# Optimization experiments

Measured on AMD Instinct MI355X. Metric: run time of the kernel, lower is better.

Reference implementation:

```python
import jax, jax.numpy as jnp
import numpy as np

B, S, D, H, FF = 2, 2048, 512, 8, 2048
DK = D // H
EPS = 1e-5


def layer_norm(x, g, b):
    mu = jnp.mean(x, axis=-1, keepdims=True)
    var = jnp.mean((x - mu) ** 2, axis=-1, keepdims=True)
    return (x - mu) / jnp.sqrt(var + EPS) * g + b


def split_heads(x):  # [B,S,D] -> [B,H,S,DK]
    b, s, _ = x.shape
    return x.reshape(b, s, H, DK).transpose(0, 2, 1, 3)


def merge_heads(x):  # [B,H,S,DK] -> [B,S,D]
    b, h, s, dk = x.shape
    return x.transpose(0, 2, 1, 3).reshape(b, s, h * dk)


def mha(q_in, kv, in_w, in_b, out_w, out_b):
    # torch nn.MultiheadAttention, batch_first, eval mode (no dropout)
    Wq, Wk, Wv = in_w[:D], in_w[D:2 * D], in_w[2 * D:]
    bq, bk, bv = in_b[:D], in_b[D:2 * D], in_b[2 * D:]
    q = split_heads(q_in @ Wq.T + bq)
    k = split_heads(kv @ Wk.T + bk)
    v = split_heads(kv @ Wv.T + bv)
    scores = jnp.einsum('bhqd,bhkd->bhqk', q, k) / jnp.sqrt(jnp.float32(DK))
    attn = jax.nn.softmax(scores, axis=-1)
    out = merge_heads(jnp.einsum('bhqk,bhkd->bhqd', attn, v))
    return out @ out_w.T + out_b


def setup_inputs() -> dict:
    key = jax.random.key(0)
    ks = jax.random.split(key, 32)
    p = lambda k, shape: (jax.random.normal(k, shape, jnp.float32) * 0.02)
    inp = {
        'x_q': jax.random.normal(ks[0], (B, S, D), jnp.float32),
        'x1': jax.random.normal(ks[1], (B, S, D), jnp.float32),
        'x2': jax.random.normal(ks[2], (B, S, D), jnp.float32),
        # causal self-attention projections (no output proj in original)
        'sa_wq': p(ks[3], (D, D)), 'sa_bq': jnp.zeros((D,), jnp.float32),
        'sa_wk': p(ks[4], (D, D)), 'sa_bk': jnp.zeros((D,), jnp.float32),
        'sa_wv': p(ks[5], (D, D)), 'sa_bv': jnp.zeros((D,), jnp.float32),
        'ln1_g': jnp.ones((D,), jnp.float32), 'ln1_b': jnp.zeros((D,), jnp.float32),
        # shared cross-attention (cross_attn used twice in forward)
        'mha_in_w': p(ks[6], (3 * D, D)), 'mha_in_b': jnp.zeros((3 * D,), jnp.float32),
        'mha_out_w': p(ks[7], (D, D)), 'mha_out_b': jnp.zeros((D,), jnp.float32),
        # shared add_norm2 (used twice)
        'ln2_g': jnp.ones((D,), jnp.float32), 'ln2_b': jnp.zeros((D,), jnp.float32),
        # FFN
        'ffn_w1': p(ks[8], (FF, D)), 'ffn_b1': jnp.zeros((FF,), jnp.float32),
        'ffn_w2': p(ks[9], (D, FF)), 'ffn_b2': jnp.zeros((D,), jnp.float32),
        # add_norm3 (final)
        'ln3_g': jnp.ones((D,), jnp.float32), 'ln3_b': jnp.zeros((D,), jnp.float32),
    }
    return inp


def reference(x_q, x1, x2, sa_wq, sa_bq, sa_wk, sa_bk, sa_wv, sa_bv,
              ln1_g, ln1_b, mha_in_w, mha_in_b, mha_out_w, mha_out_b,
              ln2_g, ln2_b, ffn_w1, ffn_b1, ffn_w2, ffn_b2, ln3_g, ln3_b):
    # --- causal self-attention (hand-rolled, masked_fill with -1e9) ---
    q = split_heads(x_q @ sa_wq.T + sa_bq)
    k = split_heads(x_q @ sa_wk.T + sa_bk)
    v = split_heads(x_q @ sa_wv.T + sa_bv)
    scores = jnp.einsum('bhqd,bhkd->bhqk', q, k) / jnp.sqrt(jnp.float32(DK))
    causal = jnp.tril(jnp.ones((S, S), dtype=bool))
    scores = jnp.where(causal[None, None], scores, jnp.float32(-1e9))
    attn = jax.nn.softmax(scores, axis=-1)
    y_sa = merge_heads(jnp.einsum('bhqk,bhkd->bhqd', attn, v))
    y = layer_norm(x_q + y_sa, ln1_g, ln1_b)
    # --- cross-attention 1 (shared weights) + shared add_norm2 ---
    yattn = mha(y, x1, mha_in_w, mha_in_b, mha_out_w, mha_out_b)
    yattn = layer_norm(y + yattn, ln2_g, ln2_b)
    # --- cross-attention 2 (SAME module/weights as cross-attn 1) ---
    yattn2 = mha(yattn, x2, mha_in_w, mha_in_b, mha_out_w, mha_out_b)
    yattn2 = layer_norm(yattn + yattn2, ln2_g, ln2_b)
    # --- FFN + add_norm3 ---
    h = jax.nn.relu(yattn2 @ ffn_w1.T + ffn_b1)
    ff = h @ ffn_w2.T + ffn_b2
    return layer_norm(yattn2 + ff, ln3_g, ln3_b)
```

## Files before the change

### kernel.cpp

```cpp
#include <hip/hip_runtime.h>
#include <hip/hip_bf16.h>

#define S_LEN 2048
#define DMODEL 512
#define NHEAD 8
#define DKH 64
#define FFDIM 2048
#define BATCH 2
#define NROWS (BATCH * S_LEN)

using bf16 = __hip_bfloat16;
typedef __bf16 bf16x8 __attribute__((ext_vector_type(8)));
typedef float floatx4 __attribute__((ext_vector_type(4)));
typedef float floatx16 __attribute__((ext_vector_type(16)));

__device__ inline unsigned short f2bf_bits(float f) {
    union { float f; unsigned u; } c; c.f = f;
    return (unsigned short)((c.u + 0x7FFFu + ((c.u >> 16) & 1u)) >> 16);
}
__device__ inline unsigned pack2bf(float a, float b) {
    return (unsigned)f2bf_bits(a) | ((unsigned)f2bf_bits(b) << 16);
}
__device__ inline unsigned pk2(float a, float b) {
    float2 f; f.x = a; f.y = b;
    __hip_bfloat162 h = __float22bfloat162_rn(f);
    return *(unsigned*)&h;
}

__device__ __forceinline__ void gload_lds16(const bf16* g, bf16* l) {
    __builtin_amdgcn_global_load_lds(
        (const __attribute__((address_space(1))) void*)(const void*)g,
        (__attribute__((address_space(3))) void*)(void*)l, 16, 0, 0);
}

struct CvtSeg { const float* s; bf16* d; int n4; };
struct CvtDesc { CvtSeg seg[12]; };

__launch_bounds__(256)
__global__ void cvt_f32_bf16(CvtDesc desc) {
    const CvtSeg sg = desc.seg[blockIdx.y];
    const int stride = gridDim.x * 256;
    for (int i = blockIdx.x * 256 + threadIdx.x; i < sg.n4; i += stride) {
        const float4 v = ((const float4*)sg.s)[i];
        uint2 o;
        o.x = pack2bf(v.x, v.y);
        o.y = pack2bf(v.z, v.w);
        ((uint2*)sg.d)[i] = o;
    }
}

struct Epi {
    bf16*  outB[3];
    float* outF[3];
    const float* bias[3];
    float scale[3];
    const bf16* A2;
    int a2slab;
    int shift;
    int relu;
};

template <int BM, int BN>
__launch_bounds__(256)
__global__ void gemm2(const bf16* __restrict__ A, const bf16* __restrict__ W,
                      Epi epi, int K)
{
    constexpr int WR = BM / 32;
    constexpr int WC = BN / 32;
    constexpr int SA = BM / 16;
    constexpr int SB = BN / 16;
    constexpr int NG = 2 * (SA + SB);

    __shared__ alignas(16) bf16 As[2][BM][32];
    __shared__ alignas(16) bf16 Bs[2][BN][32];

    const int t = threadIdx.x;
    const int w = t >> 6;
    const int lane = t & 63;
    const int r16 = lane & 15;
    const int quad = lane >> 4;
    const int wm = w >> 1, wn = w & 1;
    const int m0 = blockIdx.x * BM;
    const int n0 = blockIdx.y * BN;

    const bf16* Ause = (epi.A2 && ((n0 >> epi.shift) >= epi.a2slab)) ? epi.A2 : A;

    floatx4 acc[WR][WC];
#pragma unroll
    for (int i = 0; i < WR; i++)
#pragma unroll
        for (int j = 0; j < WC; j++)
#pragma unroll
            for (int e = 0; e < 4; e++) acc[i][j][e] = 0.0f;

    const int grow = lane >> 2;
    const int gcol = (lane & 3) * 8;

    for (int k0 = 0; k0 < K; k0 += 64) {
        __syncthreads();
#pragma unroll
        for (int s = 0; s < NG; s += 4) {
            int sg = s + w;
            int p = 0;
            if (sg >= SA + SB) { p = 1; sg -= SA + SB; }
            const bf16* src;
            bf16* dst;
            if (sg < SA) {
                src = Ause + (size_t)(m0 + sg * 16 + grow) * K + k0 + 32 * p + gcol;
                dst = &As[p][sg * 16][0] + lane * 8;
            } else {
                const int sb = sg - SA;
                src = W + (size_t)(n0 + sb * 16 + grow) * K + k0 + 32 * p + gcol;
                dst = &Bs[p][sb * 16][0] + lane * 8;
            }
            gload_lds16(src, dst);
        }
        __syncthreads();

        bf16x8 af[2][WR], bfr[2][WC];
#pragma unroll
        for (int p = 0; p < 2; p++) {
#pragma unroll
            for (int i = 0; i < WR; i++)
                af[p][i] = *(const bf16x8*)&As[p][wm * (BM / 2) + 16 * i + r16][quad * 8];
#pragma unroll
            for (int j = 0; j < WC; j++)
                bfr[p][j] = *(const bf16x8*)&Bs[p][wn * (BN / 2) + 16 * j + r16][quad * 8];
        }
#pragma unroll
        for (int p = 0; p < 2; p++)
#pragma unroll
            for (int i = 0; i < WR; i++)
#pragma unroll
                for (int j = 0; j < WC; j++)
                    acc[i][j] = __builtin_amdgcn_mfma_f32_16x16x32_bf16(af[p][i], bfr[p][j], acc[i][j], 0, 0, 0);
    }

    const int mask = (1 << epi.shift) - 1;
#pragma unroll
    for (int j = 0; j < WC; j++) {
        const int colb = n0 + wn * (BN / 2) + 16 * j;
        const int sel = __builtin_amdgcn_readfirstlane(colb >> epi.shift);
        const int lcol = (colb & mask) + r16;
        const int ldw = mask + 1;
        const float bv = epi.bias[sel] ? epi.bias[sel][lcol] : 0.0f;
        const float sc = epi.scale[sel];
        bf16* ob = epi.outB[sel];
        float* of = epi.outF[sel];
#pragma unroll
        for (int i = 0; i < WR; i++) {
            const int rowb = m0 + wm * (BM / 2) + 16 * i + 4 * quad;
#pragma unroll
            for (int e = 0; e < 4; e++) {
                float v = (acc[i][j][e] + bv) * sc;
                if (epi.relu) v = fmaxf(v, 0.0f);
                const size_t idx = (size_t)(rowb + e) * ldw + lcol;
                if (of) of[idx] = v;
                if (ob) ob[idx] = __float2bfloat16(v);
            }
        }
    }
}

#define PST 72

__launch_bounds__(512, 2)
__global__ void attn_mfma(const bf16* __restrict__ Qh, const bf16* __restrict__ Kh,
                          const bf16* __restrict__ Vh,
                          float* __restrict__ outF, bf16* __restrict__ outB,
                          int causal)
{
    __shared__ alignas(16) char smem[73728];
    typedef bf16 (*VtT)[64][PST];
    typedef bf16 (*PsT)[32][PST];
    VtT Vt = (VtT)smem;
    PsT Ps = (PsT)(smem + 36864);
    typedef float (*MshT)[2][64][34];
    MshT Msh = (MshT)smem;

    const int t = threadIdx.x;
    const int w = t >> 6;
    const int lane = t & 63;
    const int c32 = lane & 31;
    const int hi = lane >> 5;
    const int pair = t >> 7;
    const int qg = w & 1;
    const int pl = t & 127;
    const int bh = blockIdx.y;
    const int b = bh >> 3, h = bh & 7;
    const int q0 = blockIdx.x * 64;
    const size_t rowbase = (size_t)b * S_LEN;
    const int hoff = h * DKH;

    bf16x8 qf[4];
    {
        const bf16* qp = Qh + (rowbase + q0 + 32 * qg + c32) * DMODEL + hoff + 8 * hi;
#pragma unroll
        for (int tt = 0; tt < 4; tt++) qf[tt] = *(const bf16x8*)(qp + 16 * tt);
    }

    floatx16 o0, o1;
#pragma unroll
    for (int e = 0; e < 16; e++) { o0[e] = 0.0f; o1[e] = 0.0f; }
    float m = -3e38f, l = 0.0f;

    const int rq = pl & 15;
    const int c8 = ((pl >> 4) & 7) * 8;

    const int nchunk = causal ? (q0 / 64 + 1) : (S_LEN / 64);
    const int nIter = (nchunk + 3) >> 2;

    bf16x8 kf0[4], kf1[4];
    if (pair < nchunk) {
        const bf16* kp = Kh + (rowbase + pair * 64 + c32) * DMODEL + hoff + 8 * hi;
#pragma unroll
        for (int tt = 0; tt < 4; tt++) {
            kf0[tt] = *(const bf16x8*)(kp + 16 * tt);
            kf1[tt] = *(const bf16x8*)(kp + (size_t)32 * DMODEL + 16 * tt);
        }
    }

    for (int it = 0; it < nIter; it++) {
        const int ch = 4 * it + pair;
        const bool active = ch < nchunk;
        const int kb = ch * 64;
        __syncthreads();
        if (active) {
            union { uint4 u; unsigned short s[8]; } r0, r1, r2, r3;
            const bf16* vb = Vh + (rowbase + kb + 4 * rq) * DMODEL + hoff + c8;
            r0.u = *(const uint4*)(vb);
            r1.u = *(const uint4*)(vb + DMODEL);
            r2.u = *(const uint4*)(vb + 2 * DMODEL);
            r3.u = *(const uint4*)(vb + 3 * DMODEL);
#pragma unroll
            for (int j = 0; j < 8; j++) {
                ushort4 pk = { r0.s[j], r1.s[j], r2.s[j], r3.s[j] };
                *(ushort4*)&Vt[pair][c8 + j][4 * rq] = pk;
            }
        }

        if (active) {
            floatx16 s0, s1;
#pragma unroll
            for (int e = 0; e < 16; e++) { s0[e] = 0.0f; s1[e] = 0.0f; }
            __builtin_amdgcn_s_setprio(1);
#pragma unroll
            for (int tt = 0; tt < 4; tt++) {
                s0 = __builtin_amdgcn_mfma_f32_32x32x16_bf16(kf0[tt], qf[tt], s0, 0, 0, 0);
                s1 = __builtin_amdgcn_mfma_f32_32x32x16_bf16(kf1[tt], qf[tt], s1, 0, 0, 0);
            }
            __builtin_amdgcn_s_setprio(0);

            const int chn = ch + 4;
            if (chn < nchunk) {
                const bf16* kp = Kh + (rowbase + chn * 64 + c32) * DMODEL + hoff + 8 * hi;
#pragma unroll
                for (int tt = 0; tt < 4; tt++) {
                    kf0[tt] = *(const bf16x8*)(kp + 16 * tt);
                    kf1[tt] = *(const bf16x8*)(kp + (size_t)32 * DMODEL + 16 * tt);
                }
            }

            if (causal && kb == q0) {
                const int qq = 32 * qg + c32;
#pragma unroll
                for (int r = 0; r < 16; r++) {
                    const int kl = (r & 3) + 8 * (r >> 2) + 4 * hi;
                    if (kl > qq) s0[r] = -3e38f;
                    if (kl + 32 > qq) s1[r] = -3e38f;
                }
            }

            float mc = -3e38f;
#pragma unroll
            for (int r = 0; r < 16; r++) mc = fmaxf(mc, fmaxf(s0[r], s1[r]));
            mc = fmaxf(mc, __shfl_xor(mc, 32, 64));

            float alpha = 1.0f;
            if (!__all(mc <= m + 8.0f)) {
                const float mold = m;
                m = fmaxf(m, mc);
                alpha = __builtin_amdgcn_exp2f(mold - m);
#pragma unroll
                for (int r = 0; r < 16; r++) {
                    const float a = __shfl(alpha, (r & 3) + 8 * (r >> 2) + 4 * hi, 64);
                    o0[r] *= a; o1[r] *= a;
                }
            }

            float lc = 0.0f;
#pragma unroll
            for (int g = 0; g < 4; g++) {
                float p0 = __builtin_amdgcn_exp2f(s0[4 * g + 0] - m);
                float p1 = __builtin_amdgcn_exp2f(s0[4 * g + 1] - m);
                float p2 = __builtin_amdgcn_exp2f(s0[4 * g + 2] - m);
                float p3 = __builtin_amdgcn_exp2f(s0[4 * g + 3] - m);
                lc += (p0 + p1) + (p2 + p3);
                uint2 pw; pw.x = pk2(p0, p1); pw.y = pk2(p2, p3);
                *(uint2*)&Ps[w][c32][8 * g + 4 * hi] = pw;
                p0 = __builtin_amdgcn_exp2f(s1[4 * g + 0] - m);
                p1 = __builtin_amdgcn_exp2f(s1[4 * g + 1] - m);
                p2 = __builtin_amdgcn_exp2f(s1[4 * g + 2] - m);
                p3 = __builtin_amdgcn_exp2f(s1[4 * g + 3] - m);
                lc += (p0 + p1) + (p2 + p3);
                uint2 pw1; pw1.x = pk2(p0, p1); pw1.y = pk2(p2, p3);
                *(uint2*)&Ps[w][c32][32 + 8 * g + 4 * hi] = pw1;
            }
            lc += __shfl_xor(lc, 32, 64);
            l = l * alpha + lc;
        }

        __syncthreads();

        if (active) {
            __builtin_amdgcn_s_setprio(1);
#pragma unroll
            for (int tt = 0; tt < 4; tt++) {
                const bf16x8 pf = *(const bf16x8*)&Ps[w][c32][16 * tt + 8 * hi];
                const bf16x8 v0 = *(const bf16x8*)&Vt[pair][c32][16 * tt + 8 * hi];
                const bf16x8 v1 = *(const bf16x8*)&Vt[pair][32 + c32][16 * tt + 8 * hi];
                o0 = __builtin_amdgcn_mfma_f32_32x32x16_bf16(pf, v0, o0, 0, 0, 0);
                o1 = __builtin_amdgcn_mfma_f32_32x32x16_bf16(pf, v1, o1, 0, 0, 0);
            }
            __builtin_amdgcn_s_setprio(0);
        }
    }

    __syncthreads();
    if (pair & 1) {
        float* dst = &Msh[pair >> 1][qg][lane][0];
        dst[0] = m; dst[1] = l;
#pragma unroll
        for (int r = 0; r < 16; r++) { dst[2 + r] = o0[r]; dst[18 + r] = o1[r]; }
    }
    __syncthreads();
    if ((pair & 1) == 0) {
        const float* src = &Msh[pair >> 1][qg][lane][0];
        const float m_b = src[0], l_b = src[1];
        const float mt = fmaxf(m, m_b);
        const float sA = __builtin_amdgcn_exp2f(m - mt);
        const float sB = __builtin_amdgcn_exp2f(m_b - mt);
        l = l * sA + l_b * sB;
        m = mt;
#pragma unroll
        for (int r = 0; r < 16; r++) {
            const int ql = (r & 3) + 8 * (r >> 2) + 4 * hi;
            const float sAr = __shfl(sA, ql, 64);
            const float sBr = __shfl(sB, ql, 64);
            o0[r] = o0[r] * sAr + src[2 + r] * sBr;
            o1[r] = o1[r] * sAr + src[18 + r] * sBr;
        }
        if (pair == 2) {
            float* dst = &Msh[1][qg][lane][0];
            dst[0] = m; dst[1] = l;
#pragma unroll
            for (int r = 0; r < 16; r++) { dst[2 + r] = o0[r]; dst[18 + r] = o1[r]; }
        }
    }
    __syncthreads();
    if (pair == 0) {
        const float* src = &Msh[1][qg][lane][0];
        const float m_b = src[0], l_b = src[1];
        const float mt = fmaxf(m, m_b);
        const float sA = __builtin_amdgcn_exp2f(m - mt);
        const float sB = __builtin_amdgcn_exp2f(m_b - mt);
        const float lt = l * sA + l_b * sB;
#pragma unroll
        for (int r = 0; r < 16; r++) {
            const int ql = (r & 3) + 8 * (r >> 2) + 4 * hi;
            const float sAr = __shfl(sA, ql, 64);
            const float sBr = __shfl(sB, ql, 64);
            const float li = 1.0f / __shfl(lt, ql, 64);
            const float v0 = (o0[r] * sAr + src[2 + r] * sBr) * li;
            const float v1 = (o1[r] * sAr + src[18 + r] * sBr) * li;
            const size_t idx = (rowbase + q0 + 32 * qg + ql) * DMODEL + hoff + c32;
            if (outF) { outF[idx] = v0; outF[idx + 32] = v1; }
            if (outB) { outB[idx] = __float2bfloat16(v0); outB[idx + 32] = __float2bfloat16(v1); }
        }
    }
}

__launch_bounds__(256)
__global__ void ln_kernel(const float* __restrict__ xmain,
                          const float* __restrict__ resF, const bf16* __restrict__ resB,
                          const float* __restrict__ g, const float* __restrict__ bb,
                          float* __restrict__ outF, bf16* __restrict__ outB)
{
    const int row = blockIdx.x;
    const int t = threadIdx.x;
    const size_t base = (size_t)row * DMODEL;

    float x0 = xmain[base + t];
    float x1 = xmain[base + t + 256];
    if (resF) { x0 += resF[base + t]; x1 += resF[base + t + 256]; }
    if (resB) { x0 += __bfloat162float(resB[base + t]); x1 += __bfloat162float(resB[base + t + 256]); }

    __shared__ float sred[4];
    float s = x0 + x1;
#pragma unroll
    for (int off = 32; off > 0; off >>= 1) s += __shfl_down(s, off);
    if ((t & 63) == 0) sred[t >> 6] = s;
    __syncthreads();
    const float mu = (sred[0] + sred[1] + sred[2] + sred[3]) * (1.0f / DMODEL);

    const float d0 = x0 - mu, d1 = x1 - mu;
    float sv = d0 * d0 + d1 * d1;
#pragma unroll
    for (int off = 32; off > 0; off >>= 1) sv += __shfl_down(sv, off);
    __syncthreads();
    if ((t & 63) == 0) sred[t >> 6] = sv;
    __syncthreads();
    const float var = (sred[0] + sred[1] + sred[2] + sred[3]) * (1.0f / DMODEL);
    const float rstd = rsqrtf(var + 1e-5f);

    const float y0 = d0 * rstd * g[t] + bb[t];
    const float y1 = d1 * rstd * g[t + 256] + bb[t + 256];
    if (outF) { outF[base + t] = y0; outF[base + t + 256] = y1; }
    if (outB) { outB[base + t] = __float2bfloat16(y0); outB[base + t + 256] = __float2bfloat16(y1); }
}

extern "C" void kernel_launch(void* const* d_in, const int* in_sizes, int n_in,
                              void* d_out, int out_size, void* d_ws, size_t ws_size,
                              hipStream_t stream)
{
    const float* x_q       = (const float*)d_in[0];
    const float* x1        = (const float*)d_in[1];
    const float* x2        = (const float*)d_in[2];
    const float* sa_wq     = (const float*)d_in[3];
    const float* sa_bq     = (const float*)d_in[4];
    const float* sa_wk     = (const float*)d_in[5];
    const float* sa_bk     = (const float*)d_in[6];
    const float* sa_wv     = (const float*)d_in[7];
    const float* sa_bv     = (const float*)d_in[8];
    const float* ln1_g     = (const float*)d_in[9];
    const float* ln1_b     = (const float*)d_in[10];
    const float* mha_in_w  = (const float*)d_in[11];
    const float* mha_in_b  = (const float*)d_in[12];
    const float* mha_out_w = (const float*)d_in[13];
    const float* mha_out_b = (const float*)d_in[14];
    const float* ln2_g     = (const float*)d_in[15];
    const float* ln2_b     = (const float*)d_in[16];
    const float* ffn_w1    = (const float*)d_in[17];
    const float* ffn_b1    = (const float*)d_in[18];
    const float* ffn_w2    = (const float*)d_in[19];
    const float* ffn_b2    = (const float*)d_in[20];
    const float* ln3_g     = (const float*)d_in[21];
    const float* ln3_b     = (const float*)d_in[22];

    char* ws = (char*)d_ws;
    const size_t MB = 1024 * 1024;
    const size_t KB = 1024;
    bf16*  q16  = (bf16*)(ws + 0 * MB);
    bf16*  k16  = (bf16*)(ws + 4 * MB);
    bf16*  v16  = (bf16*)(ws + 8 * MB);
    bf16*  a16  = (bf16*)(ws + 12 * MB);
    float* tmp  = (float*)(ws + 16 * MB);
    bf16*  y16  = (bf16*)(ws + 24 * MB);
    bf16*  ya16 = (bf16*)(ws + 28 * MB);
    bf16*  ya2  = (bf16*)(ws + 32 * MB);
    bf16*  xq16 = (bf16*)(ws + 36 * MB);
    bf16*  x116 = (bf16*)(ws + 40 * MB);
    bf16*  x216 = (bf16*)(ws + 44 * MB);
    bf16*  w_sa_qkv = (bf16*)(ws + 48 * MB);
    bf16*  w_in   = (bf16*)(ws + 49 * MB + 512 * KB);
    bf16*  w_out  = (bf16*)(ws + 51 * MB);
    bf16*  w_f1   = (bf16*)(ws + 51 * MB + 512 * KB);
    bf16*  w_f2   = (bf16*)(ws + 53 * MB + 512 * KB);
    bf16*  h16    = (bf16*)(ws + 0 * MB);

    const int DD = DMODEL * DMODEL;
    CvtDesc cd;
    cd.seg[0]  = { x_q,       xq16,        (NROWS * DMODEL) / 4 };
    cd.seg[1]  = { x1,        x116,        (NROWS * DMODEL) / 4 };
    cd.seg[2]  = { x2,        x216,        (NROWS * DMODEL) / 4 };
    cd.seg[3]  = { sa_wq,     w_sa_qkv,           DD / 4 };
    cd.seg[4]  = { sa_wk,     w_sa_qkv + DD,      DD / 4 };
    cd.seg[5]  = { sa_wv,     w_sa_qkv + 2 * DD,  DD / 4 };
    cd.seg[6]  = { mha_in_w,  w_in,   3 * DD / 4 };
    cd.seg[7]  = { mha_out_w, w_out,  DD / 4 };
    cd.seg[8]  = { ffn_w1,    w_f1,   (FFDIM * DMODEL) / 4 };
    cd.seg[9]  = { ffn_w2,    w_f2,   (FFDIM * DMODEL) / 4 };
    cd.seg[10] = { x_q,       xq16,   0 };
    cd.seg[11] = { x_q,       xq16,   0 };
    cvt_f32_bf16<<<dim3(64, 10), 256, 0, stream>>>(cd);

    const dim3 blk(256);
    const dim3 ablk(512);
    const dim3 agrid(S_LEN / 64, BATCH * NHEAD);

    const float QSC = 0.125f * 1.44269504088896f;

    Epi eQKV = {};
    eQKV.outB[0] = q16; eQKV.outB[1] = k16; eQKV.outB[2] = v16;
    eQKV.bias[0] = sa_bq; eQKV.bias[1] = sa_bk; eQKV.bias[2] = sa_bv;
    eQKV.scale[0] = QSC; eQKV.scale[1] = 1.0f; eQKV.scale[2] = 1.0f;
    eQKV.shift = 9;

    Epi eX1 = {};
    eX1.outB[0] = q16; eX1.outB[1] = k16; eX1.outB[2] = v16;
    eX1.bias[0] = mha_in_b; eX1.bias[1] = mha_in_b + DMODEL; eX1.bias[2] = mha_in_b + 2 * DMODEL;
    eX1.scale[0] = QSC; eX1.scale[1] = 1.0f; eX1.scale[2] = 1.0f;
    eX1.A2 = x116; eX1.a2slab = 1; eX1.shift = 9;

    Epi eX2 = eX1;
    eX2.A2 = x216;

    Epi eOut = {};
    eOut.outF[0] = tmp; eOut.bias[0] = mha_out_b; eOut.scale[0] = 1.0f; eOut.shift = 9;

    Epi eF1 = {};
    eF1.outB[0] = h16; eF1.bias[0] = ffn_b1; eF1.scale[0] = 1.0f;
    eF1.shift = 11; eF1.relu = 1;

    Epi eF2 = {};
    eF2.outF[0] = tmp; eF2.bias[0] = ffn_b2; eF2.scale[0] = 1.0f; eF2.shift = 9;

    gemm2<64, 64><<<dim3(64, 24), blk, 0, stream>>>(xq16, w_sa_qkv, eQKV, DMODEL);
    attn_mfma<<<agrid, ablk, 0, stream>>>(q16, k16, v16, tmp, nullptr, 1);
    ln_kernel<<<NROWS, blk, 0, stream>>>(tmp, x_q, nullptr, ln1_g, ln1_b, nullptr, y16);

    gemm2<64, 64><<<dim3(64, 24), blk, 0, stream>>>(y16, w_in, eX1, DMODEL);
    attn_mfma<<<agrid, ablk, 0, stream>>>(q16, k16, v16, nullptr, a16, 0);
    gemm2<64, 64><<<dim3(64, 8), blk, 0, stream>>>(a16, w_out, eOut, DMODEL);
    ln_kernel<<<NROWS, blk, 0, stream>>>(tmp, nullptr, y16, ln2_g, ln2_b, nullptr, ya16);

    gemm2<64, 64><<<dim3(64, 24), blk, 0, stream>>>(ya16, w_in, eX2, DMODEL);
    attn_mfma<<<agrid, ablk, 0, stream>>>(q16, k16, v16, nullptr, a16, 0);
    gemm2<64, 64><<<dim3(64, 8), blk, 0, stream>>>(a16, w_out, eOut, DMODEL);
    ln_kernel<<<NROWS, blk, 0, stream>>>(tmp, nullptr, ya16, ln2_g, ln2_b, nullptr, ya2);

    gemm2<128, 128><<<dim3(32, 16), blk, 0, stream>>>(ya2, w_f1, eF1, DMODEL);
    gemm2<64, 64><<<dim3(64, 8), blk, 0, stream>>>(h16, w_f2, eF2, FFDIM);
    ln_kernel<<<NROWS, blk, 0, stream>>>(tmp, nullptr, ya2, ln3_g, ln3_b, (float*)d_out, nullptr);
}
```

Before: 440.6 us.

## Write V transposed from QKV GEMM epilogue and read it directly in attention

The QKV projection epilogue now stores V in a per-batch transposed [D, S] layout, so the attention kernel can load V fragments straight from global memory into registers. This removes the per-chunk LDS transpose of V, the V shared-memory buffer, and both block-wide barriers in the attention loop, letting each wave pair proceed independently. The cost is strided, uncoalesced 2-byte scattered stores in the GEMM epilogue and V fragment loads from global/L2 issued inside the loop, which are not prefetched ahead like K.

```diff
diff --git a/kernel.cpp b/kernel.cpp
--- a/kernel.cpp
+++ b/kernel.cpp
@@ -58,6 +58,7 @@
     int a2slab;
     int shift;
     int relu;
+    int vtransSel;
 };
 
 template <int BM, int BN>
@@ -150,13 +151,24 @@
 #pragma unroll
         for (int i = 0; i < WR; i++) {
             const int rowb = m0 + wm * (BM / 2) + 16 * i + 4 * quad;
-#pragma unroll
-            for (int e = 0; e < 4; e++) {
-                float v = (acc[i][j][e] + bv) * sc;
-                if (epi.relu) v = fmaxf(v, 0.0f);
-                const size_t idx = (size_t)(rowb + e) * ldw + lcol;
-                if (of) of[idx] = v;
-                if (ob) ob[idx] = __float2bfloat16(v);
+            if (sel == epi.vtransSel) {
+#pragma unroll
+                for (int e = 0; e < 4; e++) {
+                    const int row = rowb + e;
+                    const float v = (acc[i][j][e] + bv) * sc;
+                    const size_t tidx = ((size_t)(row >> 11) * DMODEL + lcol) * (size_t)S_LEN
+                                      + (row & (S_LEN - 1));
+                    ob[tidx] = __float2bfloat16(v);
+                }
+            } else {
+#pragma unroll
+                for (int e = 0; e < 4; e++) {
+                    float v = (acc[i][j][e] + bv) * sc;
+                    if (epi.relu) v = fmaxf(v, 0.0f);
+                    const size_t idx = (size_t)(rowb + e) * ldw + lcol;
+                    if (of) of[idx] = v;
+                    if (ob) ob[idx] = __float2bfloat16(v);
+                }
             }
         }
     }
@@ -166,15 +178,13 @@
 
 __launch_bounds__(512, 2)
 __global__ void attn_mfma(const bf16* __restrict__ Qh, const bf16* __restrict__ Kh,
-                          const bf16* __restrict__ Vh,
+                          const bf16* __restrict__ VTh,
                           float* __restrict__ outF, bf16* __restrict__ outB,
                           int causal)
 {
-    __shared__ alignas(16) char smem[73728];
-    typedef bf16 (*VtT)[64][PST];
+    __shared__ alignas(16) char smem[36864];
     typedef bf16 (*PsT)[32][PST];
-    VtT Vt = (VtT)smem;
-    PsT Ps = (PsT)(smem + 36864);
+    PsT Ps = (PsT)smem;
     typedef float (*MshT)[2][64][34];
     MshT Msh = (MshT)smem;
 
@@ -183,9 +193,8 @@
     const int lane = t & 63;
     const int c32 = lane & 31;
     const int hi = lane >> 5;
-    const int pair = t >> 7;
+    const int pair = w >> 1;
     const int qg = w & 1;
-    const int pl = t & 127;
     const int bh = blockIdx.y;
     const int b = bh >> 3, h = bh & 7;
     const int q0 = blockIdx.x * 64;
@@ -204,11 +213,10 @@
     for (int e = 0; e < 16; e++) { o0[e] = 0.0f; o1[e] = 0.0f; }
     float m = -3e38f, l = 0.0f;
 
-    const int rq = pl & 15;
-    const int c8 = ((pl >> 4) & 7) * 8;
-
     const int nchunk = causal ? (q0 / 64 + 1) : (S_LEN / 64);
-    const int nIter = (nchunk + 3) >> 2;
+
+    const bf16* vb0 = VTh + ((size_t)b * DMODEL + hoff + c32) * S_LEN;
+    const bf16* vb1 = VTh + ((size_t)b * DMODEL + hoff + 32 + c32) * S_LEN;
 
     bf16x8 kf0[4], kf1[4];
     if (pair < nchunk) {
@@ -220,110 +228,92 @@
         }
     }
 
-    for (int it = 0; it < nIter; it++) {
-        const int ch = 4 * it + pair;
-        const bool active = ch < nchunk;
+    for (int ch = pair; ch < nchunk; ch += 4) {
         const int kb = ch * 64;
-        __syncthreads();
-        if (active) {
-            union { uint4 u; unsigned short s[8]; } r0, r1, r2, r3;
-            const bf16* vb = Vh + (rowbase + kb + 4 * rq) * DMODEL + hoff + c8;
-            r0.u = *(const uint4*)(vb);
-            r1.u = *(const uint4*)(vb + DMODEL);
-            r2.u = *(const uint4*)(vb + 2 * DMODEL);
-            r3.u = *(const uint4*)(vb + 3 * DMODEL);
-#pragma unroll
-            for (int j = 0; j < 8; j++) {
-                ushort4 pk = { r0.s[j], r1.s[j], r2.s[j], r3.s[j] };
-                *(ushort4*)&Vt[pair][c8 + j][4 * rq] = pk;
+
+        floatx16 s0, s1;
+#pragma unroll
+        for (int e = 0; e < 16; e++) { s0[e] = 0.0f; s1[e] = 0.0f; }
+        __builtin_amdgcn_s_setprio(1);
+#pragma unroll
+        for (int tt = 0; tt < 4; tt++) {
+            s0 = __builtin_amdgcn_mfma_f32_32x32x16_bf16(kf0[tt], qf[tt], s0, 0, 0, 0);
+            s1 = __builtin_amdgcn_mfma_f32_32x32x16_bf16(kf1[tt], qf[tt], s1, 0, 0, 0);
+        }
+        __builtin_amdgcn_s_setprio(0);
+
+        if (ch + 4 < nchunk) {
+            const bf16* kp = Kh + (rowbase + (ch + 4) * 64 + c32) * DMODEL + hoff + 8 * hi;
+#pragma unroll
+            for (int tt = 0; tt < 4; tt++) {
+                kf0[tt] = *(const bf16x8*)(kp + 16 * tt);
+                kf1[tt] = *(const bf16x8*)(kp + (size_t)32 * DMODEL + 16 * tt);
             }
         }
 
-        if (active) {
-            floatx16 s0, s1;
-#pragma unroll
-            for (int e = 0; e < 16; e++) { s0[e] = 0.0f; s1[e] = 0.0f; }
-            __builtin_amdgcn_s_setprio(1);
-#pragma unroll
-            for (int tt = 0; tt < 4; tt++) {
-                s0 = __builtin_amdgcn_mfma_f32_32x32x16_bf16(kf0[tt], qf[tt], s0, 0, 0, 0);
-                s1 = __builtin_amdgcn_mfma_f32_32x32x16_bf16(kf1[tt], qf[tt], s1, 0, 0, 0);
+        if (causal && kb == q0) {
+            const int qq = 32 * qg + c32;
+#pragma unroll
+            for (int r = 0; r < 16; r++) {
+                const int kl = (r & 3) + 8 * (r >> 2) + 4 * hi;
+                if (kl > qq) s0[r] = -3e38f;
+                if (kl + 32 > qq) s1[r] = -3e38f;
             }
-            __builtin_amdgcn_s_setprio(0);
-
-            const int chn = ch + 4;
-            if (chn < nchunk) {
-                const bf16* kp = Kh + (rowbase + chn * 64 + c32) * DMODEL + hoff + 8 * hi;
-#pragma unroll
-                for (int tt = 0; tt < 4; tt++) {
-                    kf0[tt] = *(const bf16x8*)(kp + 16 * tt);
-                    kf1[tt] = *(const bf16x8*)(kp + (size_t)32 * DMODEL + 16 * tt);
-                }
+        }
+
+        float mc = -3e38f;
+#pragma unroll
+        for (int r = 0; r < 16; r++) mc = fmaxf(mc, fmaxf(s0[r], s1[r]));
+        mc = fmaxf(mc, __shfl_xor(mc, 32, 64));
+
+        float alpha = 1.0f;
+        if (!__all(mc <= m + 8.0f)) {
+            const float mold = m;
+            m = fmaxf(m, mc);
+            alpha = __builtin_amdgcn_exp2f(mold - m);
+#pragma unroll
+            for (int r = 0; r < 16; r++) {
+                const float a = __shfl(alpha, (r & 3) + 8 * (r >> 2) + 4 * hi, 64);
+                o0[r] *= a; o1[r] *= a;
             }
-
-            if (causal && kb == q0) {
-                const int qq = 32 * qg + c32;
-#pragma unroll
-                for (int r = 0; r < 16; r++) {
-                    const int kl = (r & 3) + 8 * (r >> 2) + 4 * hi;
-                    if (kl > qq) s0[r] = -3e38f;
-                    if (kl + 32 > qq) s1[r] = -3e38f;
-                }
-            }
-
-            float mc = -3e38f;
-#pragma unroll
-            for (int r = 0; r < 16; r++) mc = fmaxf(mc, fmaxf(s0[r], s1[r]));
-            mc = fmaxf(mc, __shfl_xor(mc, 32, 64));
-
-            float alpha = 1.0f;
-            if (!__all(mc <= m + 8.0f)) {
-                const float mold = m;
-                m = fmaxf(m, mc);
-                alpha = __builtin_amdgcn_exp2f(mold - m);
-#pragma unroll
-                for (int r = 0; r < 16; r++) {
-                    const float a = __shfl(alpha, (r & 3) + 8 * (r >> 2) + 4 * hi, 64);
-                    o0[r] *= a; o1[r] *= a;
-                }
-            }
-
-            float lc = 0.0f;
-#pragma unroll
-            for (int g = 0; g < 4; g++) {
-                float p0 = __builtin_amdgcn_exp2f(s0[4 * g + 0] - m);
-                float p1 = __builtin_amdgcn_exp2f(s0[4 * g + 1] - m);
-                float p2 = __builtin_amdgcn_exp2f(s0[4 * g + 2] - m);
-                float p3 = __builtin_amdgcn_exp2f(s0[4 * g + 3] - m);
-                lc += (p0 + p1) + (p2 + p3);
-                uint2 pw; pw.x = pk2(p0, p1); pw.y = pk2(p2, p3);
-                *(uint2*)&Ps[w][c32][8 * g + 4 * hi] = pw;
-                p0 = __builtin_amdgcn_exp2f(s1[4 * g + 0] - m);
-                p1 = __builtin_amdgcn_exp2f(s1[4 * g + 1] - m);
-                p2 = __builtin_amdgcn_exp2f(s1[4 * g + 2] - m);
-                p3 = __builtin_amdgcn_exp2f(s1[4 * g + 3] - m);
-                lc += (p0 + p1) + (p2 + p3);
-                uint2 pw1; pw1.x = pk2(p0, p1); pw1.y = pk2(p2, p3);
-                *(uint2*)&Ps[w][c32][32 + 8 * g + 4 * hi] = pw1;
-            }
-            lc += __shfl_xor(lc, 32, 64);
-            l = l * alpha + lc;
-        }
-
-        __syncthreads();
-
-        if (active) {
-            __builtin_amdgcn_s_setprio(1);
-#pragma unroll
-            for (int tt = 0; tt < 4; tt++) {
-                const bf16x8 pf = *(const bf16x8*)&Ps[w][c32][16 * tt + 8 * hi];
-                const bf16x8 v0 = *(const bf16x8*)&Vt[pair][c32][16 * tt + 8 * hi];
-                const bf16x8 v1 = *(const bf16x8*)&Vt[pair][32 + c32][16 * tt + 8 * hi];
-                o0 = __builtin_amdgcn_mfma_f32_32x32x16_bf16(pf, v0, o0, 0, 0, 0);
-                o1 = __builtin_amdgcn_mfma_f32_32x32x16_bf16(pf, v1, o1, 0, 0, 0);
-            }
-            __builtin_amdgcn_s_setprio(0);
-        }
+        }
+
+        float lc = 0.0f;
+#pragma unroll
+        for (int g = 0; g < 4; g++) {
+            float p0 = __builtin_amdgcn_exp2f(s0[4 * g + 0] - m);
+            float p1 = __builtin_amdgcn_exp2f(s0[4 * g + 1] - m);
+            float p2 = __builtin_amdgcn_exp2f(s0[4 * g + 2] - m);
+            float p3 = __builtin_amdgcn_exp2f(s0[4 * g + 3] - m);
+            lc += (p0 + p1) + (p2 + p3);
+            uint2 pw; pw.x = pk2(p0, p1); pw.y = pk2(p2, p3);
+            *(uint2*)&Ps[w][c32][8 * g + 4 * hi] = pw;
+            p0 = __builtin_amdgcn_exp2f(s1[4 * g + 0] - m);
+            p1 = __builtin_amdgcn_exp2f(s1[4 * g + 1] - m);
+            p2 = __builtin_amdgcn_exp2f(s1[4 * g + 2] - m);
+            p3 = __builtin_amdgcn_exp2f(s1[4 * g + 3] - m);
+            lc += (p0 + p1) + (p2 + p3);
+            uint2 pw1; pw1.x = pk2(p0, p1); pw1.y = pk2(p2, p3);
+            *(uint2*)&Ps[w][c32][32 + 8 * g + 4 * hi] = pw1;
+        }
+        lc += __shfl_xor(lc, 32, 64);
+        l = l * alpha + lc;
+
+        bf16x8 vf0[4], vf1[4];
+#pragma unroll
+        for (int tt = 0; tt < 4; tt++) {
+            vf0[tt] = *(const bf16x8*)(vb0 + kb + 16 * tt + 8 * hi);
+            vf1[tt] = *(const bf16x8*)(vb1 + kb + 16 * tt + 8 * hi);
+        }
+
+        __builtin_amdgcn_s_setprio(1);
+#pragma unroll
+        for (int tt = 0; tt < 4; tt++) {
+            const bf16x8 pf = *(const bf16x8*)&Ps[w][c32][16 * tt + 8 * hi];
+            o0 = __builtin_amdgcn_mfma_f32_32x32x16_bf16(pf, vf0[tt], o0, 0, 0, 0);
+            o1 = __builtin_amdgcn_mfma_f32_32x32x16_bf16(pf, vf1[tt], o1, 0, 0, 0);
+        }
+        __builtin_amdgcn_s_setprio(0);
     }
 
     __syncthreads();
@@ -452,7 +442,7 @@
     const size_t KB = 1024;
     bf16*  q16  = (bf16*)(ws + 0 * MB);
     bf16*  k16  = (bf16*)(ws + 4 * MB);
-    bf16*  v16  = (bf16*)(ws + 8 * MB);
+    bf16*  vT16 = (bf16*)(ws + 8 * MB);
     bf16*  a16  = (bf16*)(ws + 12 * MB);
     float* tmp  = (float*)(ws + 16 * MB);
     bf16*  y16  = (bf16*)(ws + 24 * MB);
@@ -491,41 +481,43 @@
     const float QSC = 0.125f * 1.44269504088896f;
 
     Epi eQKV = {};
-    eQKV.outB[0] = q16; eQKV.outB[1] = k16; eQKV.outB[2] = v16;
+    eQKV.outB[0] = q16; eQKV.outB[1] = k16; eQKV.outB[2] = vT16;
     eQKV.bias[0] = sa_bq; eQKV.bias[1] = sa_bk; eQKV.bias[2] = sa_bv;
     eQKV.scale[0] = QSC; eQKV.scale[1] = 1.0f; eQKV.scale[2] = 1.0f;
-    eQKV.shift = 9;
+    eQKV.shift = 9; eQKV.vtransSel = 2;
 
     Epi eX1 = {};
-    eX1.outB[0] = q16; eX1.outB[1] = k16; eX1.outB[2] = v16;
+    eX1.outB[0] = q16; eX1.outB[1] = k16; eX1.outB[2] = vT16;
     eX1.bias[0] = mha_in_b; eX1.bias[1] = mha_in_b + DMODEL; eX1.bias[2] = mha_in_b + 2 * DMODEL;
     eX1.scale[0] = QSC; eX1.scale[1] = 1.0f; eX1.scale[2] = 1.0f;
-    eX1.A2 = x116; eX1.a2slab = 1; eX1.shift = 9;
+    eX1.A2 = x116; eX1.a2slab = 1; eX1.shift = 9; eX1.vtransSel = 2;
 
     Epi eX2 = eX1;
     eX2.A2 = x216;
 
     Epi eOut = {};
     eOut.outF[0] = tmp; eOut.bias[0] = mha_out_b; eOut.scale[0] = 1.0f; eOut.shift = 9;
+    eOut.vtransSel = -1;
 
     Epi eF1 = {};
     eF1.outB[0] = h16; eF1.bias[0] = ffn_b1; eF1.scale[0] = 1.0f;
-    eF1.shift = 11; eF1.relu = 1;
+    eF1.shift = 11; eF1.relu = 1; eF1.vtransSel = -1;
 
     Epi eF2 = {};
     eF2.outF[0] = tmp; eF2.bias[0] = ffn_b2; eF2.scale[0] = 1.0f; eF2.shift = 9;
+    eF2.vtransSel = -1;
 
     gemm2<64, 64><<<dim3(64, 24), blk, 0, stream>>>(xq16, w_sa_qkv, eQKV, DMODEL);
-    attn_mfma<<<agrid, ablk, 0, stream>>>(q16, k16, v16, tmp, nullptr, 1);
+    attn_mfma<<<agrid, ablk, 0, stream>>>(q16, k16, vT16, tmp, nullptr, 1);
     ln_kernel<<<NROWS, blk, 0, stream>>>(tmp, x_q, nullptr, ln1_g, ln1_b, nullptr, y16);
 
     gemm2<64, 64><<<dim3(64, 24), blk, 0, stream>>>(y16, w_in, eX1, DMODEL);
-    attn_mfma<<<agrid, ablk, 0, stream>>>(q16, k16, v16, nullptr, a16, 0);
+    attn_mfma<<<agrid, ablk, 0, stream>>>(q16, k16, vT16, nullptr, a16, 0);
     gemm2<64, 64><<<dim3(64, 8), blk, 0, stream>>>(a16, w_out, eOut, DMODEL);
     ln_kernel<<<NROWS, blk, 0, stream>>>(tmp, nullptr, y16, ln2_g, ln2_b, nullptr, ya16);
 
     gemm2<64, 64><<<dim3(64, 24), blk, 0, stream>>>(ya16, w_in, eX2, DMODEL);
-    attn_mfma<<<agrid, ablk, 0, stream>>>(q16, k16, v16, nullptr, a16, 0);
+    attn_mfma<<<agrid, ablk, 0, stream>>>(q16, k16, vT16, nullptr, a16, 0);
     gemm2<64, 64><<<dim3(64, 8), blk, 0, stream>>>(a16, w_out, eOut, DMODEL);
     ln_kernel<<<NROWS, blk, 0, stream>>>(tmp, nullptr, ya16, ln2_g, ln2_b, nullptr, ya2);
 
```

Measured after the change: 477.6 us. 1.08x slower.

## Stage K tiles through LDS with coalesced loads instead of register prefetch

Applied to the files above, without the earlier changes.

The attention kernel now loads each 64-row K chunk with coalesced 16-byte global loads into a shared-memory tile, then reads the MFMA fragments back from LDS. The tile shares space with the P buffer, and V moves to the second half of shared memory. This targets the strided per-lane global K fragment loads. In exchange it drops the register prefetch of the next K chunk that overlapped with the softmax work, and adds barriers to each iteration while removing the one before the PV MFMA.

```diff
diff --git a/kernel.cpp b/kernel.cpp
--- a/kernel.cpp
+++ b/kernel.cpp
@@ -171,10 +171,12 @@
                           int causal)
 {
     __shared__ alignas(16) char smem[73728];
+    typedef bf16 (*KsT)[64][PST];
+    typedef bf16 (*PsT)[32][PST];
     typedef bf16 (*VtT)[64][PST];
-    typedef bf16 (*PsT)[32][PST];
-    VtT Vt = (VtT)smem;
-    PsT Ps = (PsT)(smem + 36864);
+    KsT Ks = (KsT)smem;
+    PsT Ps = (PsT)smem;
+    VtT Vt = (VtT)(smem + 36864);
     typedef float (*MshT)[2][64][34];
     MshT Msh = (MshT)smem;
 
@@ -206,26 +208,29 @@
 
     const int rq = pl & 15;
     const int c8 = ((pl >> 4) & 7) * 8;
+    const int ku = pl & 7;
+    const int kr0 = pl >> 3;
 
     const int nchunk = causal ? (q0 / 64 + 1) : (S_LEN / 64);
     const int nIter = (nchunk + 3) >> 2;
-
-    bf16x8 kf0[4], kf1[4];
-    if (pair < nchunk) {
-        const bf16* kp = Kh + (rowbase + pair * 64 + c32) * DMODEL + hoff + 8 * hi;
-#pragma unroll
-        for (int tt = 0; tt < 4; tt++) {
-            kf0[tt] = *(const bf16x8*)(kp + 16 * tt);
-            kf1[tt] = *(const bf16x8*)(kp + (size_t)32 * DMODEL + 16 * tt);
-        }
-    }
 
     for (int it = 0; it < nIter; it++) {
         const int ch = 4 * it + pair;
         const bool active = ch < nchunk;
         const int kb = ch * 64;
         __syncthreads();
+
         if (active) {
+            const bf16* kpg = Kh + (rowbase + kb + kr0) * DMODEL + hoff + ku * 8;
+            uint4 ka = *(const uint4*)(kpg);
+            uint4 kbv = *(const uint4*)(kpg + (size_t)16 * DMODEL);
+            uint4 kc = *(const uint4*)(kpg + (size_t)32 * DMODEL);
+            uint4 kd = *(const uint4*)(kpg + (size_t)48 * DMODEL);
+            *(uint4*)&Ks[pair][kr0     ][ku * 8] = ka;
+            *(uint4*)&Ks[pair][kr0 + 16][ku * 8] = kbv;
+            *(uint4*)&Ks[pair][kr0 + 32][ku * 8] = kc;
+            *(uint4*)&Ks[pair][kr0 + 48][ku * 8] = kd;
+
             union { uint4 u; unsigned short s[8]; } r0, r1, r2, r3;
             const bf16* vb = Vh + (rowbase + kb + 4 * rq) * DMODEL + hoff + c8;
             r0.u = *(const uint4*)(vb);
@@ -239,6 +244,19 @@
             }
         }
 
+        __syncthreads();
+
+        bf16x8 kf0[4], kf1[4];
+        if (active) {
+#pragma unroll
+            for (int tt = 0; tt < 4; tt++) {
+                kf0[tt] = *(const bf16x8*)&Ks[pair][c32][16 * tt + 8 * hi];
+                kf1[tt] = *(const bf16x8*)&Ks[pair][32 + c32][16 * tt + 8 * hi];
+            }
+        }
+
+        __syncthreads();
+
         if (active) {
             floatx16 s0, s1;
 #pragma unroll
@@ -250,16 +268,6 @@
                 s1 = __builtin_amdgcn_mfma_f32_32x32x16_bf16(kf1[tt], qf[tt], s1, 0, 0, 0);
             }
             __builtin_amdgcn_s_setprio(0);
-
-            const int chn = ch + 4;
-            if (chn < nchunk) {
-                const bf16* kp = Kh + (rowbase + chn * 64 + c32) * DMODEL + hoff + 8 * hi;
-#pragma unroll
-                for (int tt = 0; tt < 4; tt++) {
-                    kf0[tt] = *(const bf16x8*)(kp + 16 * tt);
-                    kf1[tt] = *(const bf16x8*)(kp + (size_t)32 * DMODEL + 16 * tt);
-                }
-            }
 
             if (causal && kb == q0) {
                 const int qq = 32 * qg + c32;
@@ -308,11 +316,7 @@
             }
             lc += __shfl_xor(lc, 32, 64);
             l = l * alpha + lc;
-        }
-
-        __syncthreads();
-
-        if (active) {
+
             __builtin_amdgcn_s_setprio(1);
 #pragma unroll
             for (int tt = 0; tt < 4; tt++) {
```

Measured after the change: 434.6 us. No clear change (-1.4%).

## Shrink attention blocks to 32 queries and make per-wave KV loop barrier-free

Applied to the files above, without the earlier changes.

The attention kernel now uses 256-thread blocks covering 32 query rows instead of 512 threads covering 64. Each wave owns its own key chunks and a private transposed-V buffer, so the per-iteration block-wide __syncthreads calls go away. V is staged in two 32-row halves, interleaved with the PV MFMAs, and the causal mask is applied only on each query tile's last chunk. The grid doubles and LDS use halves, which should raise occupancy and tighten causal load balance, at the cost of K/V being reloaded for twice as many query tiles.

```diff
diff --git a/kernel.cpp b/kernel.cpp
--- a/kernel.cpp
+++ b/kernel.cpp
@@ -163,19 +163,20 @@
 }
 
 #define PST 72
-
-__launch_bounds__(512, 2)
+#define PSTH 36
+
+__launch_bounds__(256, 4)
 __global__ void attn_mfma(const bf16* __restrict__ Qh, const bf16* __restrict__ Kh,
                           const bf16* __restrict__ Vh,
                           float* __restrict__ outF, bf16* __restrict__ outB,
                           int causal)
 {
-    __shared__ alignas(16) char smem[73728];
-    typedef bf16 (*VtT)[64][PST];
+    __shared__ alignas(16) char smem[36864];
+    typedef bf16 (*VtT)[64][PSTH];
     typedef bf16 (*PsT)[32][PST];
     VtT Vt = (VtT)smem;
-    PsT Ps = (PsT)(smem + 36864);
-    typedef float (*MshT)[2][64][34];
+    PsT Ps = (PsT)(smem + 18432);
+    typedef float (*MshT)[64][34];
     MshT Msh = (MshT)smem;
 
     const int t = threadIdx.x;
@@ -183,18 +184,15 @@
     const int lane = t & 63;
     const int c32 = lane & 31;
     const int hi = lane >> 5;
-    const int pair = t >> 7;
-    const int qg = w & 1;
-    const int pl = t & 127;
     const int bh = blockIdx.y;
     const int b = bh >> 3, h = bh & 7;
-    const int q0 = blockIdx.x * 64;
+    const int q0 = blockIdx.x * 32;
     const size_t rowbase = (size_t)b * S_LEN;
     const int hoff = h * DKH;
 
     bf16x8 qf[4];
     {
-        const bf16* qp = Qh + (rowbase + q0 + 32 * qg + c32) * DMODEL + hoff + 8 * hi;
+        const bf16* qp = Qh + (rowbase + q0 + c32) * DMODEL + hoff + 8 * hi;
 #pragma unroll
         for (int tt = 0; tt < 4; tt++) qf[tt] = *(const bf16x8*)(qp + 16 * tt);
     }
@@ -204,15 +202,14 @@
     for (int e = 0; e < 16; e++) { o0[e] = 0.0f; o1[e] = 0.0f; }
     float m = -3e38f, l = 0.0f;
 
-    const int rq = pl & 15;
-    const int c8 = ((pl >> 4) & 7) * 8;
+    const int vq = lane & 7;
+    const int vd = (lane >> 3) * 8;
 
     const int nchunk = causal ? (q0 / 64 + 1) : (S_LEN / 64);
-    const int nIter = (nchunk + 3) >> 2;
 
     bf16x8 kf0[4], kf1[4];
-    if (pair < nchunk) {
-        const bf16* kp = Kh + (rowbase + pair * 64 + c32) * DMODEL + hoff + 8 * hi;
+    if (w < nchunk) {
+        const bf16* kp = Kh + (rowbase + w * 64 + c32) * DMODEL + hoff + 8 * hi;
 #pragma unroll
         for (int tt = 0; tt < 4; tt++) {
             kf0[tt] = *(const bf16x8*)(kp + 16 * tt);
@@ -220,122 +217,142 @@
         }
     }
 
-    for (int it = 0; it < nIter; it++) {
-        const int ch = 4 * it + pair;
-        const bool active = ch < nchunk;
+    for (int ch = w; ch < nchunk; ch += 4) {
         const int kb = ch * 64;
-        __syncthreads();
-        if (active) {
+
+        floatx16 s0, s1;
+#pragma unroll
+        for (int e = 0; e < 16; e++) { s0[e] = 0.0f; s1[e] = 0.0f; }
+        __builtin_amdgcn_s_setprio(1);
+#pragma unroll
+        for (int tt = 0; tt < 4; tt++) {
+            s0 = __builtin_amdgcn_mfma_f32_32x32x16_bf16(kf0[tt], qf[tt], s0, 0, 0, 0);
+            s1 = __builtin_amdgcn_mfma_f32_32x32x16_bf16(kf1[tt], qf[tt], s1, 0, 0, 0);
+        }
+        __builtin_amdgcn_s_setprio(0);
+
+        const bf16* vb0 = Vh + (rowbase + kb + 4 * vq) * DMODEL + hoff + vd;
+        uint4 va0 = *(const uint4*)(vb0);
+        uint4 va1 = *(const uint4*)(vb0 + DMODEL);
+        uint4 va2 = *(const uint4*)(vb0 + 2 * DMODEL);
+        uint4 va3 = *(const uint4*)(vb0 + 3 * DMODEL);
+
+        if (causal && ch == nchunk - 1) {
+            const int qq = q0 + c32;
+#pragma unroll
+            for (int r = 0; r < 16; r++) {
+                const int kl = kb + (r & 3) + 8 * (r >> 2) + 4 * hi;
+                if (kl > qq) s0[r] = -3e38f;
+                if (kl + 32 > qq) s1[r] = -3e38f;
+            }
+        }
+
+        float mc = -3e38f;
+#pragma unroll
+        for (int r = 0; r < 16; r++) mc = fmaxf(mc, fmaxf(s0[r], s1[r]));
+        mc = fmaxf(mc, __shfl_xor(mc, 32, 64));
+
+        float alpha = 1.0f;
+        if (!__all(mc <= m + 8.0f)) {
+            const float mold = m;
+            m = fmaxf(m, mc);
+            alpha = __builtin_amdgcn_exp2f(mold - m);
+#pragma unroll
+            for (int r = 0; r < 16; r++) {
+                const float a = __shfl(alpha, (r & 3) + 8 * (r >> 2) + 4 * hi, 64);
+                o0[r] *= a; o1[r] *= a;
+            }
+        }
+
+        float lc = 0.0f;
+#pragma unroll
+        for (int g = 0; g < 4; g++) {
+            float p0 = __builtin_amdgcn_exp2f(s0[4 * g + 0] - m);
+            float p1 = __builtin_amdgcn_exp2f(s0[4 * g + 1] - m);
+            float p2 = __builtin_amdgcn_exp2f(s0[4 * g + 2] - m);
+            float p3 = __builtin_amdgcn_exp2f(s0[4 * g + 3] - m);
+            lc += (p0 + p1) + (p2 + p3);
+            uint2 pw; pw.x = pk2(p0, p1); pw.y = pk2(p2, p3);
+            *(uint2*)&Ps[w][c32][8 * g + 4 * hi] = pw;
+            p0 = __builtin_amdgcn_exp2f(s1[4 * g + 0] - m);
+            p1 = __builtin_amdgcn_exp2f(s1[4 * g + 1] - m);
+            p2 = __builtin_amdgcn_exp2f(s1[4 * g + 2] - m);
+            p3 = __builtin_amdgcn_exp2f(s1[4 * g + 3] - m);
+            lc += (p0 + p1) + (p2 + p3);
+            uint2 pw1; pw1.x = pk2(p0, p1); pw1.y = pk2(p2, p3);
+            *(uint2*)&Ps[w][c32][32 + 8 * g + 4 * hi] = pw1;
+        }
+        lc += __shfl_xor(lc, 32, 64);
+        l = l * alpha + lc;
+
+        if (ch + 4 < nchunk) {
+            const bf16* kp = Kh + (rowbase + (ch + 4) * 64 + c32) * DMODEL + hoff + 8 * hi;
+#pragma unroll
+            for (int tt = 0; tt < 4; tt++) {
+                kf0[tt] = *(const bf16x8*)(kp + 16 * tt);
+                kf1[tt] = *(const bf16x8*)(kp + (size_t)32 * DMODEL + 16 * tt);
+            }
+        }
+
+        {
             union { uint4 u; unsigned short s[8]; } r0, r1, r2, r3;
-            const bf16* vb = Vh + (rowbase + kb + 4 * rq) * DMODEL + hoff + c8;
-            r0.u = *(const uint4*)(vb);
-            r1.u = *(const uint4*)(vb + DMODEL);
-            r2.u = *(const uint4*)(vb + 2 * DMODEL);
-            r3.u = *(const uint4*)(vb + 3 * DMODEL);
+            r0.u = va0; r1.u = va1; r2.u = va2; r3.u = va3;
 #pragma unroll
             for (int j = 0; j < 8; j++) {
                 ushort4 pk = { r0.s[j], r1.s[j], r2.s[j], r3.s[j] };
-                *(ushort4*)&Vt[pair][c8 + j][4 * rq] = pk;
-            }
-        }
-
-        if (active) {
-            floatx16 s0, s1;
-#pragma unroll
-            for (int e = 0; e < 16; e++) { s0[e] = 0.0f; s1[e] = 0.0f; }
-            __builtin_amdgcn_s_setprio(1);
-#pragma unroll
-            for (int tt = 0; tt < 4; tt++) {
-                s0 = __builtin_amdgcn_mfma_f32_32x32x16_bf16(kf0[tt], qf[tt], s0, 0, 0, 0);
-                s1 = __builtin_amdgcn_mfma_f32_32x32x16_bf16(kf1[tt], qf[tt], s1, 0, 0, 0);
-            }
-            __builtin_amdgcn_s_setprio(0);
-
-            const int chn = ch + 4;
-            if (chn < nchunk) {
-                const bf16* kp = Kh + (rowbase + chn * 64 + c32) * DMODEL + hoff + 8 * hi;
-#pragma unroll
-                for (int tt = 0; tt < 4; tt++) {
-                    kf0[tt] = *(const bf16x8*)(kp + 16 * tt);
-                    kf1[tt] = *(const bf16x8*)(kp + (size_t)32 * DMODEL + 16 * tt);
-                }
-            }
-
-            if (causal && kb == q0) {
-                const int qq = 32 * qg + c32;
-#pragma unroll
-                for (int r = 0; r < 16; r++) {
-                    const int kl = (r & 3) + 8 * (r >> 2) + 4 * hi;
-                    if (kl > qq) s0[r] = -3e38f;
-                    if (kl + 32 > qq) s1[r] = -3e38f;
-                }
-            }
-
-            float mc = -3e38f;
-#pragma unroll
-            for (int r = 0; r < 16; r++) mc = fmaxf(mc, fmaxf(s0[r], s1[r]));
-            mc = fmaxf(mc, __shfl_xor(mc, 32, 64));
-
-            float alpha = 1.0f;
-            if (!__all(mc <= m + 8.0f)) {
-                const float mold = m;
-                m = fmaxf(m, mc);
-                alpha = __builtin_amdgcn_exp2f(mold - m);
-#pragma unroll
-                for (int r = 0; r < 16; r++) {
-                    const float a = __shfl(alpha, (r & 3) + 8 * (r >> 2) + 4 * hi, 64);
-                    o0[r] *= a; o1[r] *= a;
-                }
-            }
-
-            float lc = 0.0f;
-#pragma unroll
-            for (int g = 0; g < 4; g++) {
-                float p0 = __builtin_amdgcn_exp2f(s0[4 * g + 0] - m);
-                float p1 = __builtin_amdgcn_exp2f(s0[4 * g + 1] - m);
-                float p2 = __builtin_amdgcn_exp2f(s0[4 * g + 2] - m);
-                float p3 = __builtin_amdgcn_exp2f(s0[4 * g + 3] - m);
-                lc += (p0 + p1) + (p2 + p3);
-                uint2 pw; pw.x = pk2(p0, p1); pw.y = pk2(p2, p3);
-                *(uint2*)&Ps[w][c32][8 * g + 4 * hi] = pw;
-                p0 = __builtin_amdgcn_exp2f(s1[4 * g + 0] - m);
-                p1 = __builtin_amdgcn_exp2f(s1[4 * g + 1] - m);
-                p2 = __builtin_amdgcn_exp2f(s1[4 * g + 2] - m);
-                p3 = __builtin_amdgcn_exp2f(s1[4 * g + 3] - m);
-                lc += (p0 + p1) + (p2 + p3);
-                uint2 pw1; pw1.x = pk2(p0, p1); pw1.y = pk2(p2, p3);
-                *(uint2*)&Ps[w][c32][32 + 8 * g + 4 * hi] = pw1;
-            }
-            lc += __shfl_xor(lc, 32, 64);
-            l = l * alpha + lc;
-        }
-
-        __syncthreads();
-
-        if (active) {
-            __builtin_amdgcn_s_setprio(1);
-#pragma unroll
-            for (int tt = 0; tt < 4; tt++) {
-                const bf16x8 pf = *(const bf16x8*)&Ps[w][c32][16 * tt + 8 * hi];
-                const bf16x8 v0 = *(const bf16x8*)&Vt[pair][c32][16 * tt + 8 * hi];
-                const bf16x8 v1 = *(const bf16x8*)&Vt[pair][32 + c32][16 * tt + 8 * hi];
-                o0 = __builtin_amdgcn_mfma_f32_32x32x16_bf16(pf, v0, o0, 0, 0, 0);
-                o1 = __builtin_amdgcn_mfma_f32_32x32x16_bf16(pf, v1, o1, 0, 0, 0);
-            }
-            __builtin_amdgcn_s_setprio(0);
-        }
+                *(ushort4*)&Vt[w][vd + j][4 * vq] = pk;
+            }
+        }
+
+        const bf16* vb1 = Vh + (rowbase + kb + 32 + 4 * vq) * DMODEL + hoff + vd;
+        uint4 vc0 = *(const uint4*)(vb1);
+        uint4 vc1 = *(const uint4*)(vb1 + DMODEL);
+        uint4 vc2 = *(const uint4*)(vb1 + 2 * DMODEL);
+        uint4 vc3 = *(const uint4*)(vb1 + 3 * DMODEL);
+
+        __builtin_amdgcn_s_setprio(1);
+#pragma unroll
+        for (int tt = 0; tt < 2; tt++) {
+            const bf16x8 pf = *(const bf16x8*)&Ps[w][c32][16 * tt + 8 * hi];
+            const bf16x8 v0 = *(const bf16x8*)&Vt[w][c32][16 * tt + 8 * hi];
+            const bf16x8 v1 = *(const bf16x8*)&Vt[w][32 + c32][16 * tt + 8 * hi];
+            o0 = __builtin_amdgcn_mfma_f32_32x32x16_bf16(pf, v0, o0, 0, 0, 0);
+            o1 = __builtin_amdgcn_mfma_f32_32x32x16_bf16(pf, v1, o1, 0, 0, 0);
+        }
+        __builtin_amdgcn_s_setprio(0);
+
+        {
+            union { uint4 u; unsigned short s[8]; } r0, r1, r2, r3;
+            r0.u = vc0; r1.u = vc1; r2.u = vc2; r3.u = vc3;
+#pragma unroll
+            for (int j = 0; j < 8; j++) {
+                ushort4 pk = { r0.s[j], r1.s[j], r2.s[j], r3.s[j] };
+                *(ushort4*)&Vt[w][vd + j][4 * vq] = pk;
+            }
+        }
+
+        __builtin_amdgcn_s_setprio(1);
+#pragma unroll
+        for (int tt = 2; tt < 4; tt++) {
+            const bf16x8 pf = *(const bf16x8*)&Ps[w][c32][16 * tt + 8 * hi];
+            const bf16x8 v0 = *(const bf16x8*)&Vt[w][c32][16 * (tt - 2) + 8 * hi];
+            const bf16x8 v1 = *(const bf16x8*)&Vt[w][32 + c32][16 * (tt - 2) + 8 * hi];
+            o0 = __builtin_amdgcn_mfma_f32_32x32x16_bf16(pf, v0, o0, 0, 0, 0);
+            o1 = __builtin_amdgcn_mfma_f32_32x32x16_bf16(pf, v1, o1, 0, 0, 0);
+        }
+        __builtin_amdgcn_s_setprio(0);
     }
 
     __syncthreads();
-    if (pair & 1) {
-        float* dst = &Msh[pair >> 1][qg][lane][0];
+    if (w & 1) {
+        float* dst = &Msh[w >> 1][lane][0];
         dst[0] = m; dst[1] = l;
 #pragma unroll
         for (int r = 0; r < 16; r++) { dst[2 + r] = o0[r]; dst[18 + r] = o1[r]; }
     }
     __syncthreads();
-    if ((pair & 1) == 0) {
-        const float* src = &Msh[pair >> 1][qg][lane][0];
+    if ((w & 1) == 0) {
+        const float* src = &Msh[w >> 1][lane][0];
         const float m_b = src[0], l_b = src[1];
         const float mt = fmaxf(m, m_b);
         const float sA = __builtin_amdgcn_exp2f(m - mt);
@@ -350,16 +367,16 @@
             o0[r] = o0[r] * sAr + src[2 + r] * sBr;
             o1[r] = o1[r] * sAr + src[18 + r] * sBr;
         }
-        if (pair == 2) {
-            float* dst = &Msh[1][qg][lane][0];
+        if (w == 2) {
+            float* dst = &Msh[1][lane][0];
             dst[0] = m; dst[1] = l;
 #pragma unroll
             for (int r = 0; r < 16; r++) { dst[2 + r] = o0[r]; dst[18 + r] = o1[r]; }
         }
     }
     __syncthreads();
-    if (pair == 0) {
-        const float* src = &Msh[1][qg][lane][0];
+    if (w == 0) {
+        const float* src = &Msh[1][lane][0];
         const float m_b = src[0], l_b = src[1];
         const float mt = fmaxf(m, m_b);
         const float sA = __builtin_amdgcn_exp2f(m - mt);
@@ -373,7 +390,7 @@
             const float li = 1.0f / __shfl(lt, ql, 64);
             const float v0 = (o0[r] * sAr + src[2 + r] * sBr) * li;
             const float v1 = (o1[r] * sAr + src[18 + r] * sBr) * li;
-            const size_t idx = (rowbase + q0 + 32 * qg + ql) * DMODEL + hoff + c32;
+            const size_t idx = (rowbase + q0 + ql) * DMODEL + hoff + c32;
             if (outF) { outF[idx] = v0; outF[idx + 32] = v1; }
             if (outB) { outB[idx] = __float2bfloat16(v0); outB[idx + 32] = __float2bfloat16(v1); }
         }
@@ -485,8 +502,8 @@
     cvt_f32_bf16<<<dim3(64, 10), 256, 0, stream>>>(cd);
 
     const dim3 blk(256);
-    const dim3 ablk(512);
-    const dim3 agrid(S_LEN / 64, BATCH * NHEAD);
+    const dim3 ablk(256);
+    const dim3 agrid(S_LEN / 32, BATCH * NHEAD);
 
     const float QSC = 0.125f * 1.44269504088896f;
 
```

Result: slower. 620.4 us (+40.8%).
